# Kernel optimization log

Measured on AMD Instinct MI355X. Metric: run time of the kernel, lower is better.

Reference implementation:

```python
import jax, jax.numpy as jnp
import numpy as np

N, C, T, V = 64, 256, 64, 25

def setup_inputs() -> dict:
    key = jax.random.key(0)
    ks = jax.random.split(key, 11)
    inp = {
        't': jax.random.uniform(ks[0], (1,), dtype=jnp.float32),
        'x': jax.random.normal(ks[1], (N, C, T, V), dtype=jnp.float32),
        'A': jax.random.normal(ks[2], (V, V), dtype=jnp.float32) * 0.2,
    }
    for i in range(4):
        inp[f'w{i+1}'] = jax.random.normal(ks[3 + 2 * i], (C, C), dtype=jnp.float32) * (1.0 / np.sqrt(C))
        inp[f'b{i+1}'] = jax.random.normal(ks[4 + 2 * i], (C,), dtype=jnp.float32) * 0.02
    return inp


def _block(res, A, w, b):
    # graph diffusion over joint dim: A[v,u] @ x[n,c,t,u]
    y = jnp.einsum('vu,nctu->nctv', A, res)
    # 1x1 conv == pointwise channel GEMM
    y = jnp.einsum('oc,nctv->notv', w, y) + b[None, :, None, None]
    return jax.nn.relu(y + res)


def reference(t, x, A, w1, b1, w2, b2, w3, b3, w4, b4):
    # t is unused by the ODE function body (autonomous dynamics)
    res = _block(x, A, w1, b1)
    res = _block(res, A, w2, b2)
    res = _block(res, A, w3, b3)
    res = _block(res, A, w4, b4)
    return res
```

## Files before the change

kernel.cpp:

```cpp
#include <hip/hip_runtime.h>
#include <math.h>

#define NN 64
#define CC 256
#define TT 64
#define VV 25

typedef __bf16 bf16;
typedef __attribute__((ext_vector_type(8)))  __bf16 bf16x8;
typedef __attribute__((ext_vector_type(4)))  __bf16 bf16x4;
typedef __attribute__((ext_vector_type(16))) float  f32x16;

#define RS 40
#define YS 264
#define AS 40

__global__ void convert_w(const float* __restrict__ w1, const float* __restrict__ w2,
                          const float* __restrict__ w3, const float* __restrict__ w4,
                          bf16* __restrict__ wp) {
    const int gid = blockIdx.x * 256 + threadIdx.x;
    const int lane = gid & 63;
    const int pair = (gid >> 6) & 1;
    const int k    = (gid >> 7) & 15;
    const int wv   = (gid >> 11) & 3;
    const int blk  = gid >> 13;
    const float* src = (blk == 0) ? w1 : (blk == 1) ? w2 : (blk == 2) ? w3 : w4;
    const int row = wv * 64 + pair * 32 + (lane & 31);
    const int col = k * 16 + (lane >> 5) * 8;
    const float4 f0 = *(const float4*)(src + row * CC + col);
    const float4 f1 = *(const float4*)(src + row * CC + col + 4);
    bf16x8 o;
    o[0] = (bf16)f0.x; o[1] = (bf16)f0.y; o[2] = (bf16)f0.z; o[3] = (bf16)f0.w;
    o[4] = (bf16)f1.x; o[5] = (bf16)f1.y; o[6] = (bf16)f1.z; o[7] = (bf16)f1.w;
    *(bf16x8*)(wp + (size_t)gid * 8) = o;
}

#define MFMA(A, B, C) __builtin_amdgcn_mfma_f32_32x32x16_bf16(A, B, C, 0, 0, 0)

__global__ __launch_bounds__(256, 2) void ode_mfma(
    const float* __restrict__ x, const float* __restrict__ Amat,
    const bf16* __restrict__ wp,
    const float* __restrict__ b1, const float* __restrict__ b2,
    const float* __restrict__ b3, const float* __restrict__ b4,
    float* __restrict__ out)
{
    __shared__ bf16  sres[2][CC][RS];
    __shared__ bf16  syT [2][32][YS];
    __shared__ bf16  sAb [32][AS];
    __shared__ float sbias[4][CC];

    const int t0   = blockIdx.x * 2;
    const int n    = blockIdx.y;
    const int tid  = threadIdx.x;
    const int wave = tid >> 6;
    const int lane = tid & 63;
    const int lh   = lane >> 5;
    const int l31  = lane & 31;

    sbias[0][tid] = b1[tid];
    sbias[1][tid] = b2[tid];
    sbias[2][tid] = b3[tid];
    sbias[3][tid] = b4[tid];

    for (int i = tid; i < 32 * AS; i += 256) {
        const int v = i / AS, u = i - v * AS;
        sAb[v][u] = (v < VV && u < VV) ? (bf16)Amat[v * VV + u] : (bf16)0.f;
    }

    {
        const float* xb = x + ((size_t)n * CC * TT + t0) * VV;
        #pragma unroll
        for (int it = 0; it < 25; ++it) {
            const int g2 = tid + it * 256;
            const int c = g2 / 25;
            const int off2 = g2 - c * 25;
            const float2 f = *(const float2*)(xb + (size_t)c * TT * VV + off2 * 2);
            const int f0 = off2 * 2;
            if (f0 < 24) {
                sres[0][c][f0]     = (bf16)f.x;
                sres[0][c][f0 + 1] = (bf16)f.y;
            } else if (f0 == 24) {
                sres[0][c][24] = (bf16)f.x;
                sres[1][c][0]  = (bf16)f.y;
            } else {
                sres[1][c][f0 - 25] = (bf16)f.x;
                sres[1][c][f0 - 24] = (bf16)f.y;
            }
        }
        for (int i = tid; i < 2 * CC; i += 256) {
            const int s = i >> 8, c = i & 255;
            #pragma unroll
            for (int u = VV; u < 32; ++u) sres[s][c][u] = (bf16)0.f;
        }
    }
    __syncthreads();

    for (int blk = 0; blk < 4; ++blk) {
        {
            const bf16x8 bf0 = *(const bf16x8*)&sAb[l31][lh * 8];
            const bf16x8 bf1 = *(const bf16x8*)&sAb[l31][16 + lh * 8];
            #pragma unroll
            for (int i = 0; i < 4; ++i) {
                const int idx = wave * 4 + i;
                const int s  = idx >> 3;
                const int ct = idx & 7;
                const bf16x8 af0 = *(const bf16x8*)&sres[s][ct * 32 + l31][lh * 8];
                const bf16x8 af1 = *(const bf16x8*)&sres[s][ct * 32 + l31][16 + lh * 8];
                f32x16 d = {};
                d = MFMA(af0, bf0, d);
                d = MFMA(af1, bf1, d);
                #pragma unroll
                for (int g = 0; g < 4; ++g) {
                    bf16x4 p;
                    p[0] = (bf16)d[4 * g];     p[1] = (bf16)d[4 * g + 1];
                    p[2] = (bf16)d[4 * g + 2]; p[3] = (bf16)d[4 * g + 3];
                    *(bf16x4*)&syT[s][l31][ct * 32 + 8 * g + 4 * lh] = p;
                }
            }
        }
        __syncthreads();

        const bf16* wbase = wp + ((size_t)(blk * 4 + wave) * 16) * 1024 + lane * 8;
        const int o0 = wave * 64;

        f32x16 acc00 = {}, acc01 = {}, acc10 = {}, acc11 = {};
        #pragma unroll 4
        for (int k = 0; k < 16; ++k) {
            const int c0 = k * 16 + lh * 8;
            const bf16x8 a0 = *(const bf16x8*)(wbase + k * 1024);
            const bf16x8 a1 = *(const bf16x8*)(wbase + k * 1024 + 512);
            const bf16x8 y0 = *(const bf16x8*)&syT[0][l31][c0];
            const bf16x8 y1 = *(const bf16x8*)&syT[1][l31][c0];
            acc00 = MFMA(a0, y0, acc00);
            acc01 = MFMA(a0, y1, acc01);
            acc10 = MFMA(a1, y0, acc10);
            acc11 = MFMA(a1, y1, acc11);
        }

        const int v = l31;
        #define EPILOGUE(ACC, OT, S)                                                    \
            _Pragma("unroll")                                                           \
            for (int g = 0; g < 4; ++g) {                                               \
                const int ob = o0 + (OT) * 32 + 8 * g + 4 * lh;                         \
                const float4 bq = *(const float4*)&sbias[blk][ob];                      \
                _Pragma("unroll")                                                       \
                for (int r = 0; r < 4; ++r) {                                           \
                    const int o = ob + r;                                               \
                    float val = ACC[4 * g + r] + ((const float*)&bq)[r]                 \
                              + (float)sres[S][o][v];                                   \
                    val = fmaxf(val, 0.f);                                              \
                    if (v < VV) {                                                       \
                        if (blk < 3) sres[S][o][v] = (bf16)val;                         \
                        else out[(((size_t)n * CC + o) * TT + (t0 + (S))) * VV + v] = val; \
                    }                                                                   \
                }                                                                       \
            }
        EPILOGUE(acc00, 0, 0)
        EPILOGUE(acc01, 0, 1)
        EPILOGUE(acc10, 1, 0)
        EPILOGUE(acc11, 1, 1)
        #undef EPILOGUE
        __syncthreads();
    }
}

extern "C" void kernel_launch(void* const* d_in, const int* in_sizes, int n_in,
                              void* d_out, int out_size, void* d_ws, size_t ws_size,
                              hipStream_t stream) {
    const float* x  = (const float*)d_in[1];
    const float* A  = (const float*)d_in[2];
    const float* w1 = (const float*)d_in[3];
    const float* b1 = (const float*)d_in[4];
    const float* w2 = (const float*)d_in[5];
    const float* b2 = (const float*)d_in[6];
    const float* w3 = (const float*)d_in[7];
    const float* b3 = (const float*)d_in[8];
    const float* w4 = (const float*)d_in[9];
    const float* b4 = (const float*)d_in[10];
    float* out = (float*)d_out;
    bf16* wp = (bf16*)d_ws;

    convert_w<<<128, 256, 0, stream>>>(w1, w2, w3, w4, wp);
    dim3 grid(TT / 2, NN);
    ode_mfma<<<grid, 256, 0, stream>>>(x, A, wp, b1, b2, b3, b4, out);
}
```

Before: 411.2 us.

## Process one timestep per block to halve LDS and raise occupancy

Each block now handles a single timestep instead of two. This halves shared memory, packed into one aligned buffer of about 40KB, and the accumulator registers, so launch bounds can ask for 4 blocks per CU and the grid doubles. The A-matrix fragments are hoisted out of the block loop, and the weight-conversion kernel now does coalesced reads with scattered packed writes. In exchange, each block reloads the weights once per timestep, so global and L2 weight traffic doubles, and the x reads become scalar.

```diff
diff --git a/kernel.cpp b/kernel.cpp
--- a/kernel.cpp
+++ b/kernel.cpp
@@ -13,43 +13,50 @@
 
 #define RS 40
 #define YS 264
-#define AS 40
+
+#define OFF_SRES  0
+#define OFF_SYT   20480
+#define OFF_SAB   34208
+#define OFF_SBIAS 36256
+#define SMEM_BYTES 40352
 
 __global__ void convert_w(const float* __restrict__ w1, const float* __restrict__ w2,
                           const float* __restrict__ w3, const float* __restrict__ w4,
                           bf16* __restrict__ wp) {
     const int gid = blockIdx.x * 256 + threadIdx.x;
-    const int lane = gid & 63;
-    const int pair = (gid >> 6) & 1;
-    const int k    = (gid >> 7) & 15;
-    const int wv   = (gid >> 11) & 3;
-    const int blk  = gid >> 13;
+    const int e8  = gid * 8;
+    const int blk = e8 >> 16;
+    const int off = e8 & 65535;
+    const int row = off >> 8;
+    const int col = off & 255;
     const float* src = (blk == 0) ? w1 : (blk == 1) ? w2 : (blk == 2) ? w3 : w4;
-    const int row = wv * 64 + pair * 32 + (lane & 31);
-    const int col = k * 16 + (lane >> 5) * 8;
-    const float4 f0 = *(const float4*)(src + row * CC + col);
-    const float4 f1 = *(const float4*)(src + row * CC + col + 4);
+    const float4 f0 = *(const float4*)(src + off);
+    const float4 f1 = *(const float4*)(src + off + 4);
     bf16x8 o;
     o[0] = (bf16)f0.x; o[1] = (bf16)f0.y; o[2] = (bf16)f0.z; o[3] = (bf16)f0.w;
     o[4] = (bf16)f1.x; o[5] = (bf16)f1.y; o[6] = (bf16)f1.z; o[7] = (bf16)f1.w;
-    *(bf16x8*)(wp + (size_t)gid * 8) = o;
+    const int wv = row >> 6, pair = (row >> 5) & 1, l31 = row & 31;
+    const int k = col >> 4, lh = (col >> 3) & 1;
+    wp += (((size_t)(blk * 4 + wv) * 16 + k) * 1024) + pair * 512 + (lh * 32 + l31) * 8;
+    *(bf16x8*)wp = o;
 }
 
 #define MFMA(A, B, C) __builtin_amdgcn_mfma_f32_32x32x16_bf16(A, B, C, 0, 0, 0)
 
-__global__ __launch_bounds__(256, 2) void ode_mfma(
+__global__ __launch_bounds__(256, 4) void ode_mfma(
     const float* __restrict__ x, const float* __restrict__ Amat,
     const bf16* __restrict__ wp,
     const float* __restrict__ b1, const float* __restrict__ b2,
     const float* __restrict__ b3, const float* __restrict__ b4,
     float* __restrict__ out)
 {
-    __shared__ bf16  sres[2][CC][RS];
-    __shared__ bf16  syT [2][32][YS];
-    __shared__ bf16  sAb [32][AS];
-    __shared__ float sbias[4][CC];
+    __shared__ __attribute__((aligned(16))) char smem[SMEM_BYTES];
+    bf16*  sres  = (bf16*)(smem + OFF_SRES);
+    bf16*  syT   = (bf16*)(smem + OFF_SYT);
+    bf16*  sAb   = (bf16*)(smem + OFF_SAB);
+    float* sbias = (float*)(smem + OFF_SBIAS);
 
-    const int t0   = blockIdx.x * 2;
+    const int t    = blockIdx.x;
     const int n    = blockIdx.y;
     const int tid  = threadIdx.x;
     const int wave = tid >> 6;
@@ -57,64 +64,47 @@
     const int lh   = lane >> 5;
     const int l31  = lane & 31;
 
-    sbias[0][tid] = b1[tid];
-    sbias[1][tid] = b2[tid];
-    sbias[2][tid] = b3[tid];
-    sbias[3][tid] = b4[tid];
+    sbias[0 * CC + tid] = b1[tid];
+    sbias[1 * CC + tid] = b2[tid];
+    sbias[2 * CC + tid] = b3[tid];
+    sbias[3 * CC + tid] = b4[tid];
 
-    for (int i = tid; i < 32 * AS; i += 256) {
-        const int v = i / AS, u = i - v * AS;
-        sAb[v][u] = (v < VV && u < VV) ? (bf16)Amat[v * VV + u] : (bf16)0.f;
+    for (int i = tid; i < 32 * 32; i += 256) {
+        const int v = i >> 5, u = i & 31;
+        sAb[i] = (v < VV && u < VV) ? (bf16)Amat[v * VV + u] : (bf16)0.f;
     }
 
     {
-        const float* xb = x + ((size_t)n * CC * TT + t0) * VV;
+        const float* xb = x + ((size_t)n * CC * TT + t) * VV;
+        for (int i = tid; i < CC * VV; i += 256) {
+            const int c = i / VV;
+            const int v = i - c * VV;
+            sres[c * RS + v] = (bf16)xb[(size_t)c * TT * VV + v];
+        }
         #pragma unroll
-        for (int it = 0; it < 25; ++it) {
-            const int g2 = tid + it * 256;
-            const int c = g2 / 25;
-            const int off2 = g2 - c * 25;
-            const float2 f = *(const float2*)(xb + (size_t)c * TT * VV + off2 * 2);
-            const int f0 = off2 * 2;
-            if (f0 < 24) {
-                sres[0][c][f0]     = (bf16)f.x;
-                sres[0][c][f0 + 1] = (bf16)f.y;
-            } else if (f0 == 24) {
-                sres[0][c][24] = (bf16)f.x;
-                sres[1][c][0]  = (bf16)f.y;
-            } else {
-                sres[1][c][f0 - 25] = (bf16)f.x;
-                sres[1][c][f0 - 24] = (bf16)f.y;
-            }
-        }
-        for (int i = tid; i < 2 * CC; i += 256) {
-            const int s = i >> 8, c = i & 255;
-            #pragma unroll
-            for (int u = VV; u < 32; ++u) sres[s][c][u] = (bf16)0.f;
-        }
+        for (int u = VV; u < 32; ++u) sres[tid * RS + u] = (bf16)0.f;
     }
     __syncthreads();
 
+    const bf16x8 bfA0 = *(const bf16x8*)&sAb[l31 * 32 + lh * 8];
+    const bf16x8 bfA1 = *(const bf16x8*)&sAb[l31 * 32 + 16 + lh * 8];
+
     for (int blk = 0; blk < 4; ++blk) {
-        {
-            const bf16x8 bf0 = *(const bf16x8*)&sAb[l31][lh * 8];
-            const bf16x8 bf1 = *(const bf16x8*)&sAb[l31][16 + lh * 8];
-            #pragma unroll
-            for (int i = 0; i < 4; ++i) {
-                const int idx = wave * 4 + i;
-                const int s  = idx >> 3;
-                const int ct = idx & 7;
-                const bf16x8 af0 = *(const bf16x8*)&sres[s][ct * 32 + l31][lh * 8];
-                const bf16x8 af1 = *(const bf16x8*)&sres[s][ct * 32 + l31][16 + lh * 8];
-                f32x16 d = {};
-                d = MFMA(af0, bf0, d);
-                d = MFMA(af1, bf1, d);
+        #pragma unroll
+        for (int i = 0; i < 2; ++i) {
+            const int ct = wave * 2 + i;
+            const bf16x8 af0 = *(const bf16x8*)&sres[(ct * 32 + l31) * RS + lh * 8];
+            const bf16x8 af1 = *(const bf16x8*)&sres[(ct * 32 + l31) * RS + 16 + lh * 8];
+            f32x16 d = {};
+            d = MFMA(af0, bfA0, d);
+            d = MFMA(af1, bfA1, d);
+            if (l31 < VV) {
                 #pragma unroll
                 for (int g = 0; g < 4; ++g) {
                     bf16x4 p;
                     p[0] = (bf16)d[4 * g];     p[1] = (bf16)d[4 * g + 1];
                     p[2] = (bf16)d[4 * g + 2]; p[3] = (bf16)d[4 * g + 3];
-                    *(bf16x4*)&syT[s][l31][ct * 32 + 8 * g + 4 * lh] = p;
+                    *(bf16x4*)&syT[l31 * YS + ct * 32 + 8 * g + 4 * lh] = p;
                 }
             }
         }
@@ -123,42 +113,36 @@
         const bf16* wbase = wp + ((size_t)(blk * 4 + wave) * 16) * 1024 + lane * 8;
         const int o0 = wave * 64;
 
-        f32x16 acc00 = {}, acc01 = {}, acc10 = {}, acc11 = {};
+        f32x16 acc0 = {}, acc1 = {};
         #pragma unroll 4
         for (int k = 0; k < 16; ++k) {
-            const int c0 = k * 16 + lh * 8;
+            const bf16x8 y0 = *(const bf16x8*)&syT[l31 * YS + k * 16 + lh * 8];
             const bf16x8 a0 = *(const bf16x8*)(wbase + k * 1024);
             const bf16x8 a1 = *(const bf16x8*)(wbase + k * 1024 + 512);
-            const bf16x8 y0 = *(const bf16x8*)&syT[0][l31][c0];
-            const bf16x8 y1 = *(const bf16x8*)&syT[1][l31][c0];
-            acc00 = MFMA(a0, y0, acc00);
-            acc01 = MFMA(a0, y1, acc01);
-            acc10 = MFMA(a1, y0, acc10);
-            acc11 = MFMA(a1, y1, acc11);
+            acc0 = MFMA(a0, y0, acc0);
+            acc1 = MFMA(a1, y0, acc1);
         }
 
         const int v = l31;
-        #define EPILOGUE(ACC, OT, S)                                                    \
-            _Pragma("unroll")                                                           \
-            for (int g = 0; g < 4; ++g) {                                               \
-                const int ob = o0 + (OT) * 32 + 8 * g + 4 * lh;                         \
-                const float4 bq = *(const float4*)&sbias[blk][ob];                      \
-                _Pragma("unroll")                                                       \
-                for (int r = 0; r < 4; ++r) {                                           \
-                    const int o = ob + r;                                               \
-                    float val = ACC[4 * g + r] + ((const float*)&bq)[r]                 \
-                              + (float)sres[S][o][v];                                   \
-                    val = fmaxf(val, 0.f);                                              \
-                    if (v < VV) {                                                       \
-                        if (blk < 3) sres[S][o][v] = (bf16)val;                         \
-                        else out[(((size_t)n * CC + o) * TT + (t0 + (S))) * VV + v] = val; \
-                    }                                                                   \
-                }                                                                       \
+        #define EPILOGUE(ACC, OT)                                                   \
+            _Pragma("unroll")                                                       \
+            for (int g = 0; g < 4; ++g) {                                           \
+                const int ob = o0 + (OT) * 32 + 8 * g + 4 * lh;                     \
+                const float4 bq = *(const float4*)&sbias[blk * CC + ob];            \
+                _Pragma("unroll")                                                   \
+                for (int r = 0; r < 4; ++r) {                                       \
+                    const int o = ob + r;                                           \
+                    float val = ACC[4 * g + r] + ((const float*)&bq)[r]             \
+                              + (float)sres[o * RS + v];                            \
+                    val = fmaxf(val, 0.f);                                          \
+                    if (v < VV) {                                                   \
+                        if (blk < 3) sres[o * RS + v] = (bf16)val;                  \
+                        else out[(((size_t)n * CC + o) * TT + t) * VV + v] = val;   \
+                    }                                                               \
+                }                                                                   \
             }
-        EPILOGUE(acc00, 0, 0)
-        EPILOGUE(acc01, 0, 1)
-        EPILOGUE(acc10, 1, 0)
-        EPILOGUE(acc11, 1, 1)
+        EPILOGUE(acc0, 0)
+        EPILOGUE(acc1, 1)
         #undef EPILOGUE
         __syncthreads();
     }
@@ -181,6 +165,6 @@
     bf16* wp = (bf16*)d_ws;
 
     convert_w<<<128, 256, 0, stream>>>(w1, w2, w3, w4, wp);
-    dim3 grid(TT / 2, NN);
+    dim3 grid(TT, NN);
     ode_mfma<<<grid, 256, 0, stream>>>(x, A, wp, b1, b2, b3, b4, out);
 }
```

Measured after the change: 380.0 us. -7.6%, faster.
